# Performance work log

Measured on AMD Instinct MI355X. Metric: run time of the kernel, lower is better.

The kernel has to match this reference:

```python
import jax, jax.numpy as jnp
import numpy as np

EPS = 1e-5  # torch BatchNorm2d default eps


def _conv(x, w, b, pad):
    y = jax.lax.conv_general_dilated(
        x, w, window_strides=(1, 1), padding=[(pad, pad), (pad, pad)],
        dimension_numbers=('NCHW', 'OIHW', 'NCHW'))
    return y + b[None, :, None, None]


def _bn_train(x, gamma, beta):
    # training-mode BatchNorm2d: biased batch statistics over (N,H,W)
    m = jnp.mean(x, axis=(0, 2, 3), keepdims=True)
    v = jnp.var(x, axis=(0, 2, 3), keepdims=True)
    xn = (x - m) * jax.lax.rsqrt(v + EPS)
    return xn * gamma[None, :, None, None] + beta[None, :, None, None]


def _ncc(s, t):
    # Vectorized equivalent of the per-pixel double loop.
    # ncc[b,0,i,j] = mean(tt * ss / (tt_std * ss_std)) over (C,th,tw)
    #             = sum(tt * s_sub) / (N * tt_std * ss_std)   (since sum(tt)=0)
    b, c, sh, sw = s.shape
    th, tw = t.shape[2], t.shape[3]
    N = c * th * tw
    tt = t - jnp.mean(t, axis=(1, 2, 3), keepdims=True)
    # torch.std is unbiased (divides by N-1)
    tt_std = jnp.sqrt(jnp.sum(tt * tt, axis=(1, 2, 3), keepdims=True) / (N - 1))

    # cross[b] = valid correlation of s[b] with its own template tt[b]
    def per_sample(si, ti):
        return jax.lax.conv_general_dilated(
            si[None], ti[None], (1, 1), 'VALID',
            dimension_numbers=('NCHW', 'OIHW', 'NCHW'))[0]  # (1,h,w)

    cross = jax.vmap(per_sample)(s, tt)  # (b,1,h,w)

    # per-window mean/std of s via box-filter conv over all C channels jointly
    box = jnp.ones((1, c, th, tw), dtype=s.dtype)
    win_sum = jax.lax.conv_general_dilated(
        s, box, (1, 1), 'VALID', dimension_numbers=('NCHW', 'OIHW', 'NCHW'))
    win_sqsum = jax.lax.conv_general_dilated(
        s * s, box, (1, 1), 'VALID', dimension_numbers=('NCHW', 'OIHW', 'NCHW'))
    win_mean = win_sum / N
    ss_var = jnp.maximum(win_sqsum - N * win_mean * win_mean, 0.0) / (N - 1)
    ss_std = jnp.sqrt(ss_var)

    return cross / (N * tt_std * ss_std)  # (b,1,h,w)


def reference(s, t, w1, b1, g1, be1, w2, b2, g2, be2,
              w3, b3, g3, be3, w4, b4):
    s = _bn_train(_conv(s, w1, b1, pad=1), g1, be1)
    t = _bn_train(_conv(t, w2, b2, pad=1), g2, be2)
    ncc = _ncc(s, t)
    x = _bn_train(_conv(ncc, w3, b3, pad=0), g3, be3)
    x = jax.nn.relu(x)
    return _conv(x, w4, b4, pad=0)  # (b,2,h,w)


def setup_inputs() -> dict:
    key = jax.random.key(0)
    ks = jax.random.split(key, 12)
    C = 256
    inp = {
        's': jax.random.normal(ks[0], (16, C, 64, 64), jnp.float32),
        't': jax.random.normal(ks[1], (16, C, 16, 16), jnp.float32),
        'w1': jax.random.normal(ks[2], (C, C, 3, 3), jnp.float32) * 0.02,
        'b1': jax.random.normal(ks[3], (C,), jnp.float32) * 0.02,
        'g1': jnp.ones((C,), jnp.float32),
        'be1': jnp.zeros((C,), jnp.float32),
        'w2': jax.random.normal(ks[4], (C, C, 3, 3), jnp.float32) * 0.02,
        'b2': jax.random.normal(ks[5], (C,), jnp.float32) * 0.02,
        'g2': jnp.ones((C,), jnp.float32),
        'be2': jnp.zeros((C,), jnp.float32),
        'w3': jax.random.normal(ks[6], (1, 1, 1, 1), jnp.float32),
        'b3': jax.random.normal(ks[7], (1,), jnp.float32) * 0.02,
        'g3': jnp.ones((1,), jnp.float32),
        'be3': jnp.zeros((1,), jnp.float32),
        'w4': jax.random.normal(ks[8], (2, 1, 1, 1), jnp.float32),
        'b4': jax.random.normal(ks[9], (2,), jnp.float32) * 0.02,
    }
    return inp
```

## Files before the change

kernel.cpp:

```cpp
#include <hip/hip_runtime.h>
#include <hip/hip_bf16.h>

#define EPSV 1e-5f

constexpr int B_ = 16, C_ = 256;
constexpr int OHW_ = 49 * 49;
constexpr int NTOT = 256 * 16 * 16;
constexpr int GROUPS = 32, CPERG = 8;

typedef short bf16x8 __attribute__((ext_vector_type(8)));
typedef float f32x4 __attribute__((ext_vector_type(4)));

constexpr size_t OFF_S1 = 0;
constexpr size_t SZ_S1  = (size_t)16 * 256 * 4096;
constexpr size_t OFF_T2 = OFF_S1 + SZ_S1;
constexpr size_t SZ_T2  = (size_t)16 * 256 * 256;
constexpr size_t OFF_ST = OFF_T2 + SZ_T2;
constexpr size_t OFF_Z  = OFF_ST + 2048;
constexpr size_t OFF_C  = OFF_Z + 131072;
constexpr size_t SPC_BYTES = (size_t)16 * 66 * 66 * 256 * 2;
constexpr size_t TPC_BYTES = (size_t)16 * 18 * 18 * 256 * 2;
constexpr size_t WR_BYTES  = (size_t)9 * 256 * 256 * 2;
constexpr size_t CPOFF = 0;
constexpr size_t NCOFF = CPOFF + (size_t)GROUPS * 16 * OHW_;
constexpr size_t SATOFF = NCOFF + (size_t)16 * OHW_;

__device__ __forceinline__ void gload_lds16(const void* g, void* l) {
    __builtin_amdgcn_global_load_lds((const __attribute__((address_space(1))) unsigned int*)g,
                                     (__attribute__((address_space(3))) unsigned int*)l,
                                     16, 0, 0);
}

template<int W>
__device__ __forceinline__ void pad_body(int bid, const float* __restrict__ in,
                                         __hip_bfloat16* __restrict__ outp, float* tile)
{
    constexpr int PW = W + 2;
    int icg = bid & 3; bid >>= 2;
    int yp = bid % PW; bid /= PW;
    int b = bid;
    int ic0 = icg * 64;
    int tid = threadIdx.x;
    bool interior = (yp >= 1 && yp <= W);
    if (interior) {
        int y = yp - 1;
        for (int idx = tid; idx < 64 * W; idx += 256) {
            int i = idx / W, x = idx % W;
            tile[i * (W + 1) + x] = in[(((size_t)(b * C_ + ic0 + i)) * W + y) * W + x];
        }
    }
    __syncthreads();
    for (int idx = tid; idx < PW * 16; idx += 256) {
        int xp = idx >> 4, i4 = idx & 15;
        ushort4 v = make_ushort4(0, 0, 0, 0);
        if (interior && xp >= 1 && xp <= W) {
            #pragma unroll
            for (int k = 0; k < 4; ++k) {
                __hip_bfloat16 h = __float2bfloat16(tile[(i4 * 4 + k) * (W + 1) + xp - 1]);
                reinterpret_cast<unsigned short*>(&v)[k] = *reinterpret_cast<unsigned short*>(&h);
            }
        }
        *reinterpret_cast<ushort4*>(&outp[(((size_t)(b * PW) + yp) * PW + xp) * 256 + ic0 + i4 * 4]) = v;
    }
}

__global__ __launch_bounds__(256)
void pad_all(const float* __restrict__ s, const float* __restrict__ t,
             __hip_bfloat16* __restrict__ SPc, __hip_bfloat16* __restrict__ TPc,
             const float* __restrict__ w1, const float* __restrict__ w2,
             __hip_bfloat16* __restrict__ wr1, __hip_bfloat16* __restrict__ wr2)
{
    __shared__ float tile[64 * 65];
    constexpr int NP1 = 16 * 66 * 4, NP2 = 16 * 18 * 4;
    int bid = blockIdx.x;
    if (bid < NP1) { pad_body<64>(bid, s, SPc, tile); return; }
    bid -= NP1;
    if (bid < NP2) { pad_body<16>(bid, t, TPc, tile); return; }
    bid -= NP2;
    const float* w = (bid < 256) ? w1 : w2;
    __hip_bfloat16* wr = (bid < 256) ? wr1 : wr2;
    int idx = (bid & 255) * 256 + threadIdx.x;
    const float* src = w + (size_t)idx * 9;
    #pragma unroll
    for (int t_ = 0; t_ < 9; ++t_)
        wr[(size_t)t_ * 65536 + idx] = __float2bfloat16(src[t_]);
}

template<int W>
__device__ __forceinline__ void conv_body(
    int logical,
    const __hip_bfloat16* __restrict__ SPc, const __hip_bfloat16* __restrict__ Wr,
    const float* __restrict__ bias, float* __restrict__ out,
    float* __restrict__ csum, float* __restrict__ csq,
    __hip_bfloat16* A_lds, __hip_bfloat16* B_lds)
{
    constexpr int PW = W + 2;
    constexpr int NPIX = W * W;
    constexpr int NT = NPIX / 128;
    int nt = logical % NT; logical /= NT;
    int mt = logical & 1;  logical >>= 1;
    int b  = logical;
    int tid = threadIdx.x;
    int lane = tid & 63;
    int wv = tid >> 6, wm = wv >> 1, wn = wv & 1;
    int oc0 = mt * 128, p0 = nt * 128;

    f32x4 acc[4][4];
    #pragma unroll
    for (int i = 0; i < 4; ++i)
        #pragma unroll
        for (int j = 0; j < 4; ++j)
            #pragma unroll
            for (int r = 0; r < 4; ++r) acc[i][j][r] = 0.f;

    const bf16x8* Af = reinterpret_cast<const bf16x8*>(A_lds);
    const bf16x8* Bf = reinterpret_cast<const bf16x8*>(B_lds);
    int colb = lane >> 4;
    int rA = lane & 15;

    for (int kc = 0; kc < 72; ++kc) {
        int tap = kc >> 3, icc = kc & 7;
        int ic0 = icc * 32;
        int dy = tap / 3, dx = tap - dy * 3;
        __syncthreads();
        #pragma unroll
        for (int it = 0; it < 2; ++it) {
            int sIdx = tid + it * 256;
            int row = sIdx >> 2, seg = sIdx & 3;
            const __hip_bfloat16* srcA =
                Wr + ((size_t)(tap * 256 + oc0 + row)) * 256 + ic0 + seg * 8;
            gload_lds16(srcA, &A_lds[sIdx * 8]);
            int p = p0 + row;
            int y = p / W, x = p % W;
            const __hip_bfloat16* srcB =
                SPc + (((size_t)(b * PW + y + dy)) * PW + x + dx) * 256 + ic0 + seg * 8;
            gload_lds16(srcB, &B_lds[sIdx * 8]);
        }
        asm volatile("s_waitcnt vmcnt(0)" ::: "memory");
        __syncthreads();

        bf16x8 a[4], bb[4];
        #pragma unroll
        for (int mi = 0; mi < 4; ++mi)
            a[mi] = Af[(wm * 64 + mi * 16 + rA) * 4 + colb];
        #pragma unroll
        for (int ni = 0; ni < 4; ++ni)
            bb[ni] = Bf[(wn * 64 + ni * 16 + rA) * 4 + colb];
        #pragma unroll
        for (int mi = 0; mi < 4; ++mi)
            #pragma unroll
            for (int ni = 0; ni < 4; ++ni)
                acc[mi][ni] = __builtin_amdgcn_mfma_f32_16x16x32_bf16(
                    a[mi], bb[ni], acc[mi][ni], 0, 0, 0);
    }

    #pragma unroll
    for (int mi = 0; mi < 4; ++mi) {
        int ocb = oc0 + wm * 64 + mi * 16 + colb * 4;
        #pragma unroll
        for (int r = 0; r < 4; ++r) {
            int oc = ocb + r;
            float bv = bias[oc];
            float* orow = out + ((size_t)(b * C_ + oc)) * NPIX;
            float s_oc = 0.f, q_oc = 0.f;
            #pragma unroll
            for (int ni = 0; ni < 4; ++ni) {
                int px = p0 + wn * 64 + ni * 16 + rA;
                float v = acc[mi][ni][r] + bv;
                orow[px] = v;
                s_oc += v; q_oc += v * v;
            }
            #pragma unroll
            for (int m_ = 1; m_ < 16; m_ <<= 1) {
                s_oc += __shfl_xor(s_oc, m_);
                q_oc += __shfl_xor(q_oc, m_);
            }
            if (rA == 0) {
                atomicAdd(&csum[oc], s_oc);
                atomicAdd(&csq[oc], q_oc);
            }
        }
    }
}

__global__ __launch_bounds__(256)
void conv_all(const __hip_bfloat16* __restrict__ SPc, const __hip_bfloat16* __restrict__ Wr1,
              const float* __restrict__ b1, float* __restrict__ S1,
              float* __restrict__ CHS1, float* __restrict__ CHQ1,
              const __hip_bfloat16* __restrict__ TPc, const __hip_bfloat16* __restrict__ Wr2,
              const float* __restrict__ b2, float* __restrict__ T2,
              float* __restrict__ CHS2, float* __restrict__ CHQ2)
{
    __shared__ __hip_bfloat16 A_lds[4096];
    __shared__ __hip_bfloat16 B_lds[4096];
    int bid = blockIdx.x;
    if (bid < 64) {
        conv_body<16>(bid, TPc, Wr2, b2, T2, CHS2, CHQ2, A_lds, B_lds);
    } else {
        int l = bid - 64;
        int logical = (l & 7) * 128 + (l >> 3);
        conv_body<64>(logical, SPc, Wr1, b1, S1, CHS1, CHQ1, A_lds, B_lds);
    }
}

__device__ inline void blk_reduce2(float& a, float& q, int tid) {
    #pragma unroll
    for (int off = 32; off > 0; off >>= 1) {
        a += __shfl_down(a, off);
        q += __shfl_down(q, off);
    }
    __shared__ float ra[4], rq[4];
    if ((tid & 63) == 0) { ra[tid >> 6] = a; rq[tid >> 6] = q; }
    __syncthreads();
    if (tid == 0) { a = ra[0] + ra[1] + ra[2] + ra[3]; q = rq[0] + rq[1] + rq[2] + rq[3]; }
}

__global__ __launch_bounds__(256)
void bn_t2_stats(float* __restrict__ T2, const float* __restrict__ csum,
                 const float* __restrict__ csq, const float* __restrict__ g2,
                 const float* __restrict__ be2, float* __restrict__ tmean,
                 float* __restrict__ ttstd)
{
    __shared__ float SC[256], SH[256];
    int b = blockIdx.x, tid = threadIdx.x;
    {
        float m = csum[tid] * (1.f / 4096.f);
        float v = csq[tid] * (1.f / 4096.f) - m * m;
        float sc = rsqrtf(v + EPSV) * g2[tid];
        SC[tid] = sc; SH[tid] = be2[tid] - m * sc;
    }
    __syncthreads();
    float4* p = reinterpret_cast<float4*>(T2 + (size_t)b * NTOT);
    float s = 0.f, q = 0.f;
    for (int i4 = tid; i4 < NTOT / 4; i4 += 256) {
        int c = i4 >> 6;
        float sc = SC[c], sh = SH[c];
        float4 v = p[i4];
        v.x = v.x * sc + sh; v.y = v.y * sc + sh;
        v.z = v.z * sc + sh; v.w = v.w * sc + sh;
        s += v.x + v.y + v.z + v.w;
        q += v.x * v.x + v.y * v.y + v.z * v.z + v.w * v.w;
        p[i4] = v;
    }
    blk_reduce2(s, q, tid);
    if (tid == 0) {
        float m = s / (float)NTOT;
        tmean[b] = m;
        ttstd[b] = sqrtf(fmaxf(q - (float)NTOT * m * m, 0.f) / (float)(NTOT - 1));
    }
}

__global__ __launch_bounds__(256, 2)
void cross_v3(const float* __restrict__ s1, const float* __restrict__ t2,
              const float* __restrict__ csum, const float* __restrict__ csq,
              const float* __restrict__ g1, const float* __restrict__ be1,
              float* __restrict__ cpart, float* __restrict__ z)
{
    __shared__ float4 spl4[1024];
    __shared__ float tpl[256];
    __shared__ float red[4][64][49];

    int g = blockIdx.x & (GROUPS - 1);
    int b = blockIdx.x / GROUPS;
    int tid = threadIdx.x;
    int phase = tid >> 6;
    int lane = tid & 63;
    int i = lane;
    int i_ld = i < 49 ? i : 48;

    float acc[49];
    #pragma unroll
    for (int j = 0; j < 49; ++j) acc[j] = 0.f;
    float4 zs[4], zq[4];
    #pragma unroll
    for (int k = 0; k < 4; ++k) {
        zs[k] = make_float4(0.f, 0.f, 0.f, 0.f);
        zq[k] = make_float4(0.f, 0.f, 0.f, 0.f);
    }

    #pragma unroll 1
    for (int cc = 0; cc < CPERG; ++cc) {
        int c = g * CPERG + cc;
        float m = csum[c] * (1.f / 65536.f);
        float v = csq[c] * (1.f / 65536.f) - m * m;
        float sc = rsqrtf(v + EPSV) * g1[c];
        float sh = be1[c] - m * sc;
        __syncthreads();
        const float4* sp4 = reinterpret_cast<const float4*>(s1 + ((size_t)(b * C_ + c)) * 4096);
        #pragma unroll
        for (int k = 0; k < 4; ++k) {
            int gidx = tid + k * 256;
            float4 val = sp4[gidx];
            val.x = val.x * sc + sh; val.y = val.y * sc + sh;
            val.z = val.z * sc + sh; val.w = val.w * sc + sh;
            zs[k].x += val.x; zs[k].y += val.y; zs[k].z += val.z; zs[k].w += val.w;
            zq[k].x += val.x * val.x; zq[k].y += val.y * val.y;
            zq[k].z += val.z * val.z; zq[k].w += val.w * val.w;
            int row = gidx >> 4, jg = gidx & 15;
            spl4[row * 16 + (jg ^ (row & 7))] = val;
        }
        tpl[tid] = t2[((size_t)(b * C_ + c)) * 256 + tid];
        __syncthreads();
        #pragma unroll 1
        for (int tyl = 0; tyl < 4; ++tyl) {
            int ty = phase * 4 + tyl;
            int row = i_ld + ty;
            float r_[64];
            #pragma unroll
            for (int jg = 0; jg < 16; ++jg) {
                float4 v4 = spl4[row * 16 + (jg ^ (row & 7))];
                r_[jg * 4 + 0] = v4.x; r_[jg * 4 + 1] = v4.y;
                r_[jg * 4 + 2] = v4.z; r_[jg * 4 + 3] = v4.w;
            }
            float tt[16];
            const float4* tp4 = reinterpret_cast<const float4*>(&tpl[ty * 16]);
            #pragma unroll
            for (int k = 0; k < 4; ++k) {
                float4 tv = tp4[k];
                tt[k * 4 + 0] = tv.x; tt[k * 4 + 1] = tv.y;
                tt[k * 4 + 2] = tv.z; tt[k * 4 + 3] = tv.w;
            }
            #pragma unroll
            for (int tx = 0; tx < 16; ++tx)
                #pragma unroll
                for (int j = 0; j < 49; ++j)
                    acc[j] += tt[tx] * r_[j + tx];
        }
    }
    #pragma unroll
    for (int k = 0; k < 4; ++k) {
        int pxb = (tid + k * 256) * 4;
        float* zb  = z + (size_t)b * 4096 + pxb;
        float* z2b = z + 65536 + (size_t)b * 4096 + pxb;
        atomicAdd(&zb[0], zs[k].x);  atomicAdd(&zb[1], zs[k].y);
        atomicAdd(&zb[2], zs[k].z);  atomicAdd(&zb[3], zs[k].w);
        atomicAdd(&z2b[0], zq[k].x); atomicAdd(&z2b[1], zq[k].y);
        atomicAdd(&z2b[2], zq[k].z); atomicAdd(&z2b[3], zq[k].w);
    }
    __syncthreads();
    if (i < 49) {
        #pragma unroll
        for (int j = 0; j < 49; ++j) red[phase][i][j] = acc[j];
    }
    __syncthreads();
    float* dst = cpart + ((size_t)(g * B_ + b)) * OHW_;
    for (int e = tid; e < OHW_; e += 256) {
        int ii = e / 49, jj = e - ii * 49;
        dst[e] = red[0][ii][jj] + red[1][ii][jj] + red[2][ii][jj] + red[3][ii][jj];
    }
}

__global__ __launch_bounds__(256)
void sat_kernel(const float* __restrict__ zin, float* __restrict__ sat)
{
    __shared__ float t[65][66];
    int pl = blockIdx.x;
    int tid = threadIdx.x;
    const float* src = zin + (size_t)pl * 4096;
    for (int idx = tid; idx < 4096; idx += 256) {
        int y = idx >> 6, x = idx & 63;
        t[y + 1][x + 1] = src[idx];
    }
    for (int idx = tid; idx < 65; idx += 256) { t[0][idx] = 0.f; t[idx][0] = 0.f; }
    __syncthreads();
    if (tid < 64) {
        float run = 0.f;
        for (int x = 1; x <= 64; ++x) { run += t[tid + 1][x]; t[tid + 1][x] = run; }
    }
    __syncthreads();
    if (tid < 64) {
        float run = 0.f;
        for (int y = 1; y <= 64; ++y) { run += t[y][tid + 1]; t[y][tid + 1] = run; }
    }
    __syncthreads();
    float* dst = sat + (size_t)pl * 4225;
    for (int idx = tid; idx < 4225; idx += 256) {
        int r = idx / 65, c = idx % 65;
        dst[idx] = t[r][c];
    }
}

__global__ __launch_bounds__(256)
void ncc_kernel(const float* __restrict__ cpart, const float* __restrict__ sat,
                const float* __restrict__ tmean, const float* __restrict__ ttstd,
                float* __restrict__ ncc, float* __restrict__ s3)
{
    int idx = blockIdx.x * 256 + threadIdx.x;
    float val = 0.f;
    if (idx < B_ * OHW_) {
        int b = idx / OHW_, r = idx - b * OHW_;
        int i = r / 49, j = r - i * 49;
        float cr = 0.f;
        #pragma unroll 4
        for (int g = 0; g < GROUPS; ++g) cr += cpart[((size_t)(g * B_ + b)) * OHW_ + r];
        const float* sz = sat + (size_t)b * 4225;
        const float* sq = sat + (size_t)(16 + b) * 4225;
        int a00 = i * 65 + j, a01 = i * 65 + j + 16;
        int a10 = (i + 16) * 65 + j, a11 = (i + 16) * 65 + j + 16;
        float wsum = sz[a11] - sz[a01] - sz[a10] + sz[a00];
        float wq   = sq[a11] - sq[a01] - sq[a10] + sq[a00];
        float crosst = cr - tmean[b] * wsum;
        float ssvar = fmaxf(wq - wsum * wsum * (1.f / 65536.f), 0.f) * (1.f / 65535.f);
        float ssstd = sqrtf(ssvar);
        val = crosst / (65536.f * ttstd[b] * ssstd);
        ncc[idx] = val;
    }
    float s = val, q = val * val;
    blk_reduce2(s, q, threadIdx.x);
    if (threadIdx.x == 0) { atomicAdd(&s3[0], s); atomicAdd(&s3[1], q); }
}

__global__ __launch_bounds__(256)
void final_kernel(const float* __restrict__ ncc, const float* __restrict__ s3,
                  const float* __restrict__ w3, const float* __restrict__ b3,
                  const float* __restrict__ g3, const float* __restrict__ be3,
                  const float* __restrict__ w4, const float* __restrict__ b4,
                  float* __restrict__ out)
{
    int idx = blockIdx.x * 256 + threadIdx.x;
    if (idx >= B_ * OHW_) return;
    constexpr float M = (float)(B_ * OHW_);
    float mn = s3[0] / M;
    float vn = s3[1] / M - mn * mn;
    float W3 = w3[0], B3 = b3[0];
    float my = W3 * mn + B3;
    float vy = W3 * W3 * vn;
    float sc = rsqrtf(vy + EPSV) * g3[0];
    float y = (W3 * ncc[idx] + B3 - my) * sc + be3[0];
    float h = fmaxf(y, 0.f);
    int b = idx / OHW_, r = idx - b * OHW_;
    out[((size_t)(b * 2 + 0)) * OHW_ + r] = h * w4[0] + b4[0];
    out[((size_t)(b * 2 + 1)) * OHW_ + r] = h * w4[1] + b4[1];
}

extern "C" void kernel_launch(void* const* d_in, const int* in_sizes, int n_in,
                              void* d_out, int out_size, void* d_ws, size_t ws_size,
                              hipStream_t stream)
{
    const float* s   = (const float*)d_in[0];
    const float* t   = (const float*)d_in[1];
    const float* w1  = (const float*)d_in[2];
    const float* b1  = (const float*)d_in[3];
    const float* g1  = (const float*)d_in[4];
    const float* be1 = (const float*)d_in[5];
    const float* w2  = (const float*)d_in[6];
    const float* b2  = (const float*)d_in[7];
    const float* g2  = (const float*)d_in[8];
    const float* be2 = (const float*)d_in[9];
    const float* w3  = (const float*)d_in[10];
    const float* b3  = (const float*)d_in[11];
    const float* g3  = (const float*)d_in[12];
    const float* be3 = (const float*)d_in[13];
    const float* w4  = (const float*)d_in[14];
    const float* b4  = (const float*)d_in[15];

    float* ws = (float*)d_ws;
    float* S1 = ws + OFF_S1;
    float* T2 = ws + OFF_T2;
    float* ST = ws + OFF_ST;
    float* CHS1 = ST + 0;
    float* CHQ1 = ST + 256;
    float* CHS2 = ST + 512;
    float* CHQ2 = ST + 768;
    float* S3   = ST + 1024;
    float* TM   = ST + 1040;
    float* TSD  = ST + 1056;
    float* Z    = ws + OFF_Z;

    char* Cb = (char*)(ws + OFF_C);
    __hip_bfloat16* SPc = (__hip_bfloat16*)Cb;
    __hip_bfloat16* TPc = (__hip_bfloat16*)(Cb + SPC_BYTES);
    __hip_bfloat16* Wr1 = (__hip_bfloat16*)(Cb + SPC_BYTES + TPC_BYTES);
    __hip_bfloat16* Wr2 = (__hip_bfloat16*)(Cb + SPC_BYTES + TPC_BYTES + WR_BYTES);
    float* Cf = (float*)Cb;
    float* CP  = Cf + CPOFF;
    float* NC  = Cf + NCOFF;
    float* SAT = Cf + SATOFF;

    hipMemsetAsync(ST, 0, (2048 + 131072) * sizeof(float), stream);

    pad_all<<<dim3(16 * 66 * 4 + 16 * 18 * 4 + 512), dim3(256), 0, stream>>>(
        s, t, SPc, TPc, w1, w2, Wr1, Wr2);

    conv_all<<<dim3(64 + 1024), dim3(256), 0, stream>>>(SPc, Wr1, b1, S1, CHS1, CHQ1,
                                                        TPc, Wr2, b2, T2, CHS2, CHQ2);

    bn_t2_stats<<<dim3(16), dim3(256), 0, stream>>>(T2, CHS2, CHQ2, g2, be2, TM, TSD);

    cross_v3<<<dim3(16 * GROUPS), dim3(256), 0, stream>>>(S1, T2, CHS1, CHQ1, g1, be1, CP, Z);
    sat_kernel<<<dim3(32), dim3(256), 0, stream>>>(Z, SAT);
    ncc_kernel<<<dim3(151), dim3(256), 0, stream>>>(CP, SAT, TM, TSD, NC, S3);
    final_kernel<<<dim3(151), dim3(256), 0, stream>>>(NC, S3, w3, b3, g3, be3, w4, b4, (float*)d_out);
}
```

Measured before the change: 438.9 us.

## Rewrite conv GEMM as 256x256 tile, 8-wave, double-buffered swizzled LDS pipeline

Replaces the 128x128, 4-wave conv kernel, which waited on a full load before every K step, with a 256x256 output tile computed by 8 waves. Global-to-LDS loads for the next K step are double-buffered and interleaved with MFMA quadrants using partial vmcnt waits and raw barriers. LDS rows are XOR-swizzled to avoid bank conflicts, and s_setprio raises priority during the MFMA blocks. The trade is 128KB of dynamic LDS per block, many more accumulator registers, and only 272 blocks, which may leave the grid poorly balanced across CUs.

```diff
diff --git a/kernel.cpp b/kernel.cpp
--- a/kernel.cpp
+++ b/kernel.cpp
@@ -87,86 +87,163 @@
 }
 
 template<int W>
-__device__ __forceinline__ void conv_body(
-    int logical,
+__device__ __forceinline__ void conv8p_body(
+    int bb, int nt,
     const __hip_bfloat16* __restrict__ SPc, const __hip_bfloat16* __restrict__ Wr,
     const float* __restrict__ bias, float* __restrict__ out,
-    float* __restrict__ csum, float* __restrict__ csq,
-    __hip_bfloat16* A_lds, __hip_bfloat16* B_lds)
+    float* __restrict__ csum, float* __restrict__ csq, char* smem)
 {
     constexpr int PW = W + 2;
     constexpr int NPIX = W * W;
-    constexpr int NT = NPIX / 128;
-    int nt = logical % NT; logical /= NT;
-    int mt = logical & 1;  logical >>= 1;
-    int b  = logical;
+    constexpr int LOG2W = (W == 64) ? 6 : 4;
     int tid = threadIdx.x;
     int lane = tid & 63;
-    int wv = tid >> 6, wm = wv >> 1, wn = wv & 1;
-    int oc0 = mt * 128, p0 = nt * 128;
-
-    f32x4 acc[4][4];
-    #pragma unroll
-    for (int i = 0; i < 4; ++i)
+    int wv = tid >> 6;
+    int wm = wv >> 2, wn = wv & 3;
+    int rA = lane & 15, colb = lane >> 4;
+
+    f32x4 acc[8][4];
+    #pragma unroll
+    for (int i = 0; i < 8; ++i)
         #pragma unroll
         for (int j = 0; j < 4; ++j)
             #pragma unroll
             for (int r = 0; r < 4; ++r) acc[i][j][r] = 0.f;
 
-    const bf16x8* Af = reinterpret_cast<const bf16x8*>(A_lds);
-    const bf16x8* Bf = reinterpret_cast<const bf16x8*>(B_lds);
-    int colb = lane >> 4;
-    int rA = lane & 15;
-
-    for (int kc = 0; kc < 72; ++kc) {
-        int tap = kc >> 3, icc = kc & 7;
-        int ic0 = icc * 32;
+    int row_s[2], gs_s[2];
+    #pragma unroll
+    for (int k = 0; k < 2; ++k) {
+        int si = tid + k * 512;
+        int row = si >> 3, g = si & 7;
+        row_s[k] = row; gs_s[k] = g ^ (row & 7);
+    }
+
+    auto Abase = [&](int s, int half) { return smem + s * 32768 + half * 16384; };
+    auto Bbase = [&](int s, int half) { return smem + 65536 + s * 32768 + half * 16384; };
+
+    auto stageA = [&](int s, int half, int kt) {
+        int tap = kt >> 2, icc = kt & 3;
+        char* dst = Abase(s, half);
+        #pragma unroll
+        for (int k = 0; k < 2; ++k) {
+            const __hip_bfloat16* src =
+                Wr + ((size_t)(tap * 256 + half * 128 + row_s[k])) * 256 + icc * 64 + gs_s[k] * 8;
+            gload_lds16(src, dst + (tid + k * 512) * 16);
+        }
+    };
+    auto stageB = [&](int s, int half, int kt) {
+        int tap = kt >> 2, icc = kt & 3;
         int dy = tap / 3, dx = tap - dy * 3;
-        __syncthreads();
-        #pragma unroll
-        for (int it = 0; it < 2; ++it) {
-            int sIdx = tid + it * 256;
-            int row = sIdx >> 2, seg = sIdx & 3;
-            const __hip_bfloat16* srcA =
-                Wr + ((size_t)(tap * 256 + oc0 + row)) * 256 + ic0 + seg * 8;
-            gload_lds16(srcA, &A_lds[sIdx * 8]);
-            int p = p0 + row;
-            int y = p / W, x = p % W;
-            const __hip_bfloat16* srcB =
-                SPc + (((size_t)(b * PW + y + dy)) * PW + x + dx) * 256 + ic0 + seg * 8;
-            gload_lds16(srcB, &B_lds[sIdx * 8]);
-        }
-        asm volatile("s_waitcnt vmcnt(0)" ::: "memory");
-        __syncthreads();
-
-        bf16x8 a[4], bb[4];
-        #pragma unroll
-        for (int mi = 0; mi < 4; ++mi)
-            a[mi] = Af[(wm * 64 + mi * 16 + rA) * 4 + colb];
-        #pragma unroll
-        for (int ni = 0; ni < 4; ++ni)
-            bb[ni] = Bf[(wn * 64 + ni * 16 + rA) * 4 + colb];
-        #pragma unroll
-        for (int mi = 0; mi < 4; ++mi)
-            #pragma unroll
-            for (int ni = 0; ni < 4; ++ni)
-                acc[mi][ni] = __builtin_amdgcn_mfma_f32_16x16x32_bf16(
-                    a[mi], bb[ni], acc[mi][ni], 0, 0, 0);
-    }
-
-    #pragma unroll
-    for (int mi = 0; mi < 4; ++mi) {
-        int ocb = oc0 + wm * 64 + mi * 16 + colb * 4;
+        char* dst = Bbase(s, half);
+        #pragma unroll
+        for (int k = 0; k < 2; ++k) {
+            int row = row_s[k];
+            int gy = nt * (256 >> LOG2W) + ((half * 128 + row) >> LOG2W) + dy;
+            int gx = (row & (W - 1)) + dx;
+            const __hip_bfloat16* src =
+                SPc + (((size_t)(bb * PW + gy)) * PW + gx) * 256 + icc * 64 + gs_s[k] * 8;
+            gload_lds16(src, dst + (tid + k * 512) * 16);
+        }
+    };
+
+    bf16x8 a[4][2];
+    bf16x8 bfr[2][2][2];
+    auto loadA = [&](int s, int half) {
+        const bf16x8* Av = (const bf16x8*)Abase(s, half);
+        #pragma unroll
+        for (int mi = 0; mi < 4; ++mi) {
+            int rl = wm * 64 + mi * 16 + rA;
+            #pragma unroll
+            for (int ks = 0; ks < 2; ++ks)
+                a[mi][ks] = Av[rl * 8 + ((ks * 4 + colb) ^ (rA & 7))];
+        }
+    };
+    auto loadB0 = [&](int s) {
+        const bf16x8* Bv = (const bf16x8*)Bbase(s, 0);
+        #pragma unroll
+        for (int ni = 0; ni < 2; ++ni) {
+            int rl = wn * 32 + ni * 16 + rA;
+            #pragma unroll
+            for (int ks = 0; ks < 2; ++ks)
+                bfr[0][ni][ks] = Bv[rl * 8 + ((ks * 4 + colb) ^ (rA & 7))];
+        }
+    };
+    auto loadB1 = [&](int s) {
+        const bf16x8* Bv = (const bf16x8*)Bbase(s, 1);
+        #pragma unroll
+        for (int ni = 0; ni < 2; ++ni) {
+            int rl = wn * 32 + ni * 16 + rA;
+            #pragma unroll
+            for (int ks = 0; ks < 2; ++ks)
+                bfr[1][ni][ks] = Bv[rl * 8 + ((ks * 4 + colb) ^ (rA & 7))];
+        }
+    };
+
+    #define QUAD(mh, nh)                                                            \
+        __builtin_amdgcn_s_setprio(1);                                              \
+        _Pragma("unroll")                                                           \
+        for (int mi = 0; mi < 4; ++mi)                                              \
+            _Pragma("unroll")                                                       \
+            for (int ni = 0; ni < 2; ++ni)                                          \
+                _Pragma("unroll")                                                   \
+                for (int ks = 0; ks < 2; ++ks)                                      \
+                    acc[(mh)*4+mi][(nh)*2+ni] = __builtin_amdgcn_mfma_f32_16x16x32_bf16( \
+                        a[mi][ks], bfr[nh][ni][ks], acc[(mh)*4+mi][(nh)*2+ni], 0,0,0);   \
+        __builtin_amdgcn_s_setprio(0);
+
+    stageA(0, 0, 0); stageB(0, 0, 0); stageB(0, 1, 0); stageA(0, 1, 0);
+    asm volatile("s_waitcnt vmcnt(4)" ::: "memory");
+    asm volatile("s_barrier" ::: "memory");
+
+    for (int kt = 0; kt < 36; ++kt) {
+        int s = kt & 1, sn = s ^ 1;
+        bool st = (kt < 35);
+        int nkt = kt + 1;
+        loadA(s, 0); loadB0(s);
+        if (st) {
+            stageA(sn, 0, nkt);
+            asm volatile("s_waitcnt vmcnt(4)" ::: "memory");
+        } else {
+            asm volatile("s_waitcnt vmcnt(2)" ::: "memory");
+        }
+        asm volatile("s_barrier" ::: "memory");
+        QUAD(0, 0)
+        loadB1(s);
+        if (st) {
+            stageB(sn, 0, nkt);
+            asm volatile("s_waitcnt vmcnt(4)" ::: "memory");
+        } else {
+            asm volatile("s_waitcnt vmcnt(0)" ::: "memory");
+        }
+        asm volatile("s_barrier" ::: "memory");
+        QUAD(0, 1)
+        loadA(s, 1);
+        if (st) stageB(sn, 1, nkt);
+        asm volatile("s_barrier" ::: "memory");
+        QUAD(1, 0)
+        if (st) {
+            stageA(sn, 1, nkt);
+            asm volatile("s_waitcnt vmcnt(4)" ::: "memory");
+        }
+        asm volatile("s_barrier" ::: "memory");
+        QUAD(1, 1)
+    }
+    #undef QUAD
+
+    int p0g = nt * 256;
+    #pragma unroll
+    for (int mi = 0; mi < 8; ++mi) {
+        int oc = (mi >> 2) * 128 + wm * 64 + (mi & 3) * 16 + colb * 4;
         #pragma unroll
         for (int r = 0; r < 4; ++r) {
-            int oc = ocb + r;
-            float bv = bias[oc];
-            float* orow = out + ((size_t)(b * C_ + oc)) * NPIX;
+            int ocr = oc + r;
+            float bv = bias[ocr];
+            float* orow = out + ((size_t)(bb * C_ + ocr)) * NPIX;
             float s_oc = 0.f, q_oc = 0.f;
             #pragma unroll
-            for (int ni = 0; ni < 4; ++ni) {
-                int px = p0 + wn * 64 + ni * 16 + rA;
-                float v = acc[mi][ni][r] + bv;
+            for (int nj = 0; nj < 4; ++nj) {
+                int px = p0g + (nj >> 1) * 128 + wn * 32 + (nj & 1) * 16 + rA;
+                float v = acc[mi][nj][r] + bv;
                 orow[px] = v;
                 s_oc += v; q_oc += v * v;
             }
@@ -176,30 +253,29 @@
                 q_oc += __shfl_xor(q_oc, m_);
             }
             if (rA == 0) {
-                atomicAdd(&csum[oc], s_oc);
-                atomicAdd(&csq[oc], q_oc);
+                atomicAdd(&csum[ocr], s_oc);
+                atomicAdd(&csq[ocr], q_oc);
             }
         }
     }
 }
 
-__global__ __launch_bounds__(256)
-void conv_all(const __hip_bfloat16* __restrict__ SPc, const __hip_bfloat16* __restrict__ Wr1,
-              const float* __restrict__ b1, float* __restrict__ S1,
-              float* __restrict__ CHS1, float* __restrict__ CHQ1,
-              const __hip_bfloat16* __restrict__ TPc, const __hip_bfloat16* __restrict__ Wr2,
-              const float* __restrict__ b2, float* __restrict__ T2,
-              float* __restrict__ CHS2, float* __restrict__ CHQ2)
-{
-    __shared__ __hip_bfloat16 A_lds[4096];
-    __shared__ __hip_bfloat16 B_lds[4096];
+__global__ __launch_bounds__(512, 2)
+void conv8p(const __hip_bfloat16* __restrict__ SPc, const __hip_bfloat16* __restrict__ Wr1,
+            const float* __restrict__ b1, float* __restrict__ S1,
+            float* __restrict__ CHS1, float* __restrict__ CHQ1,
+            const __hip_bfloat16* __restrict__ TPc, const __hip_bfloat16* __restrict__ Wr2,
+            const float* __restrict__ b2, float* __restrict__ T2,
+            float* __restrict__ CHS2, float* __restrict__ CHQ2)
+{
+    extern __shared__ char smem[];
     int bid = blockIdx.x;
-    if (bid < 64) {
-        conv_body<16>(bid, TPc, Wr2, b2, T2, CHS2, CHQ2, A_lds, B_lds);
+    if (bid < 16) {
+        conv8p_body<16>(bid, 0, TPc, Wr2, b2, T2, CHS2, CHQ2, smem);
     } else {
-        int l = bid - 64;
-        int logical = (l & 7) * 128 + (l >> 3);
-        conv_body<64>(logical, SPc, Wr1, b1, S1, CHS1, CHQ1, A_lds, B_lds);
+        int l = bid - 16;
+        int logical = (l & 7) * 32 + (l >> 3);
+        conv8p_body<64>(logical >> 4, logical & 15, SPc, Wr1, b1, S1, CHS1, CHQ1, smem);
     }
 }
 
@@ -482,8 +558,10 @@
     pad_all<<<dim3(16 * 66 * 4 + 16 * 18 * 4 + 512), dim3(256), 0, stream>>>(
         s, t, SPc, TPc, w1, w2, Wr1, Wr2);
 
-    conv_all<<<dim3(64 + 1024), dim3(256), 0, stream>>>(SPc, Wr1, b1, S1, CHS1, CHQ1,
-                                                        TPc, Wr2, b2, T2, CHS2, CHQ2);
+    (void)hipFuncSetAttribute((const void*)conv8p,
+                              hipFuncAttributeMaxDynamicSharedMemorySize, 131072);
+    conv8p<<<dim3(16 + 256), dim3(512), 131072, stream>>>(SPc, Wr1, b1, S1, CHS1, CHQ1,
+                                                          TPc, Wr2, b2, T2, CHS2, CHQ2);
 
     bn_t2_stats<<<dim3(16), dim3(256), 0, stream>>>(T2, CHS2, CHQ2, g2, be2, TM, TSD);
 
```

Result: slower. 456.1 us (+3.9%).

## Store conv1 output as bf16 and fold template BN stats into cross kernel

Applied to the files above, without the earlier changes.

The large conv1 output S1 is now written in bf16 instead of fp32, which halves its write traffic in the conv kernel and its read traffic in the cross-correlation kernel. The separate bn_t2_stats launch is removed. Its per-sample mean/std computation now runs in 16 extra blocks of the cross kernel, and the T2 normalization is applied on the fly when the template is loaded, so T2 is no longer rewritten. The cost is bf16 rounding of S1 before BN and the NCC statistics, which could affect accuracy.

```diff
diff --git a/kernel.cpp b/kernel.cpp
--- a/kernel.cpp
+++ b/kernel.cpp
@@ -10,10 +10,11 @@
 
 typedef short bf16x8 __attribute__((ext_vector_type(8)));
 typedef float f32x4 __attribute__((ext_vector_type(4)));
+typedef unsigned short ushort8v __attribute__((ext_vector_type(8)));
 
 constexpr size_t OFF_S1 = 0;
-constexpr size_t SZ_S1  = (size_t)16 * 256 * 4096;
-constexpr size_t OFF_T2 = OFF_S1 + SZ_S1;
+constexpr size_t SZ_S1F = (size_t)16 * 256 * 4096 / 2;
+constexpr size_t OFF_T2 = OFF_S1 + SZ_S1F;
 constexpr size_t SZ_T2  = (size_t)16 * 256 * 256;
 constexpr size_t OFF_ST = OFF_T2 + SZ_T2;
 constexpr size_t OFF_Z  = OFF_ST + 2048;
@@ -30,6 +31,9 @@
                                      (__attribute__((address_space(3))) unsigned int*)l,
                                      16, 0, 0);
 }
+
+__device__ __forceinline__ void store_val(float* p, float v) { *p = v; }
+__device__ __forceinline__ void store_val(__hip_bfloat16* p, float v) { *p = __float2bfloat16(v); }
 
 template<int W>
 __device__ __forceinline__ void pad_body(int bid, const float* __restrict__ in,
@@ -86,11 +90,11 @@
         wr[(size_t)t_ * 65536 + idx] = __float2bfloat16(src[t_]);
 }
 
-template<int W>
+template<int W, typename OT>
 __device__ __forceinline__ void conv_body(
     int logical,
     const __hip_bfloat16* __restrict__ SPc, const __hip_bfloat16* __restrict__ Wr,
-    const float* __restrict__ bias, float* __restrict__ out,
+    const float* __restrict__ bias, OT* __restrict__ out,
     float* __restrict__ csum, float* __restrict__ csq,
     __hip_bfloat16* A_lds, __hip_bfloat16* B_lds)
 {
@@ -161,13 +165,13 @@
         for (int r = 0; r < 4; ++r) {
             int oc = ocb + r;
             float bv = bias[oc];
-            float* orow = out + ((size_t)(b * C_ + oc)) * NPIX;
+            OT* orow = out + ((size_t)(b * C_ + oc)) * NPIX;
             float s_oc = 0.f, q_oc = 0.f;
             #pragma unroll
             for (int ni = 0; ni < 4; ++ni) {
                 int px = p0 + wn * 64 + ni * 16 + rA;
                 float v = acc[mi][ni][r] + bv;
-                orow[px] = v;
+                store_val(&orow[px], v);
                 s_oc += v; q_oc += v * v;
             }
             #pragma unroll
@@ -185,7 +189,7 @@
 
 __global__ __launch_bounds__(256)
 void conv_all(const __hip_bfloat16* __restrict__ SPc, const __hip_bfloat16* __restrict__ Wr1,
-              const float* __restrict__ b1, float* __restrict__ S1,
+              const float* __restrict__ b1, __hip_bfloat16* __restrict__ S1,
               float* __restrict__ CHS1, float* __restrict__ CHQ1,
               const __hip_bfloat16* __restrict__ TPc, const __hip_bfloat16* __restrict__ Wr2,
               const float* __restrict__ b2, float* __restrict__ T2,
@@ -195,11 +199,11 @@
     __shared__ __hip_bfloat16 B_lds[4096];
     int bid = blockIdx.x;
     if (bid < 64) {
-        conv_body<16>(bid, TPc, Wr2, b2, T2, CHS2, CHQ2, A_lds, B_lds);
+        conv_body<16, float>(bid, TPc, Wr2, b2, T2, CHS2, CHQ2, A_lds, B_lds);
     } else {
         int l = bid - 64;
         int logical = (l & 7) * 128 + (l >> 3);
-        conv_body<64>(logical, SPc, Wr1, b1, S1, CHS1, CHQ1, A_lds, B_lds);
+        conv_body<64, __hip_bfloat16>(logical, SPc, Wr1, b1, S1, CHS1, CHQ1, A_lds, B_lds);
     }
 }
 
@@ -215,54 +219,52 @@
     if (tid == 0) { a = ra[0] + ra[1] + ra[2] + ra[3]; q = rq[0] + rq[1] + rq[2] + rq[3]; }
 }
 
-__global__ __launch_bounds__(256)
-void bn_t2_stats(float* __restrict__ T2, const float* __restrict__ csum,
-                 const float* __restrict__ csq, const float* __restrict__ g2,
-                 const float* __restrict__ be2, float* __restrict__ tmean,
-                 float* __restrict__ ttstd)
-{
-    __shared__ float SC[256], SH[256];
-    int b = blockIdx.x, tid = threadIdx.x;
-    {
-        float m = csum[tid] * (1.f / 4096.f);
-        float v = csq[tid] * (1.f / 4096.f) - m * m;
-        float sc = rsqrtf(v + EPSV) * g2[tid];
-        SC[tid] = sc; SH[tid] = be2[tid] - m * sc;
-    }
-    __syncthreads();
-    float4* p = reinterpret_cast<float4*>(T2 + (size_t)b * NTOT);
-    float s = 0.f, q = 0.f;
-    for (int i4 = tid; i4 < NTOT / 4; i4 += 256) {
-        int c = i4 >> 6;
-        float sc = SC[c], sh = SH[c];
-        float4 v = p[i4];
-        v.x = v.x * sc + sh; v.y = v.y * sc + sh;
-        v.z = v.z * sc + sh; v.w = v.w * sc + sh;
-        s += v.x + v.y + v.z + v.w;
-        q += v.x * v.x + v.y * v.y + v.z * v.z + v.w * v.w;
-        p[i4] = v;
-    }
-    blk_reduce2(s, q, tid);
-    if (tid == 0) {
-        float m = s / (float)NTOT;
-        tmean[b] = m;
-        ttstd[b] = sqrtf(fmaxf(q - (float)NTOT * m * m, 0.f) / (float)(NTOT - 1));
-    }
-}
-
 __global__ __launch_bounds__(256, 2)
-void cross_v3(const float* __restrict__ s1, const float* __restrict__ t2,
-              const float* __restrict__ csum, const float* __restrict__ csq,
+void cross_v4(const __hip_bfloat16* __restrict__ s1, const float* __restrict__ t2,
+              const float* __restrict__ cs1, const float* __restrict__ cq1,
               const float* __restrict__ g1, const float* __restrict__ be1,
-              float* __restrict__ cpart, float* __restrict__ z)
-{
+              const float* __restrict__ cs2, const float* __restrict__ cq2,
+              const float* __restrict__ g2, const float* __restrict__ be2,
+              float* __restrict__ cpart, float* __restrict__ z,
+              float* __restrict__ tmean, float* __restrict__ ttstd)
+{
+    int tid = threadIdx.x;
+    if (blockIdx.x >= 16 * GROUPS) {
+        __shared__ float SC[256], SH[256];
+        int b = blockIdx.x - 16 * GROUPS;
+        {
+            float m = cs2[tid] * (1.f / 4096.f);
+            float v = cq2[tid] * (1.f / 4096.f) - m * m;
+            float sc = rsqrtf(v + EPSV) * g2[tid];
+            SC[tid] = sc; SH[tid] = be2[tid] - m * sc;
+        }
+        __syncthreads();
+        const float4* p = reinterpret_cast<const float4*>(t2 + (size_t)b * NTOT);
+        float s = 0.f, q = 0.f;
+        for (int i4 = tid; i4 < NTOT / 4; i4 += 256) {
+            int c = i4 >> 6;
+            float sc = SC[c], sh = SH[c];
+            float4 v = p[i4];
+            float vx = v.x * sc + sh, vy = v.y * sc + sh;
+            float vz = v.z * sc + sh, vw = v.w * sc + sh;
+            s += vx + vy + vz + vw;
+            q += vx * vx + vy * vy + vz * vz + vw * vw;
+        }
+        blk_reduce2(s, q, tid);
+        if (tid == 0) {
+            float m = s / (float)NTOT;
+            tmean[b] = m;
+            ttstd[b] = sqrtf(fmaxf(q - (float)NTOT * m * m, 0.f) / (float)(NTOT - 1));
+        }
+        return;
+    }
+
     __shared__ float4 spl4[1024];
     __shared__ float tpl[256];
     __shared__ float red[4][64][49];
 
     int g = blockIdx.x & (GROUPS - 1);
     int b = blockIdx.x / GROUPS;
-    int tid = threadIdx.x;
     int phase = tid >> 6;
     int lane = tid & 63;
     int i = lane;
@@ -271,35 +273,42 @@
     float acc[49];
     #pragma unroll
     for (int j = 0; j < 49; ++j) acc[j] = 0.f;
-    float4 zs[4], zq[4];
-    #pragma unroll
-    for (int k = 0; k < 4; ++k) {
-        zs[k] = make_float4(0.f, 0.f, 0.f, 0.f);
-        zq[k] = make_float4(0.f, 0.f, 0.f, 0.f);
-    }
+    float zsA[2][8], zqA[2][8];
+    #pragma unroll
+    for (int k = 0; k < 2; ++k)
+        #pragma unroll
+        for (int e = 0; e < 8; ++e) { zsA[k][e] = 0.f; zqA[k][e] = 0.f; }
 
     #pragma unroll 1
     for (int cc = 0; cc < CPERG; ++cc) {
         int c = g * CPERG + cc;
-        float m = csum[c] * (1.f / 65536.f);
-        float v = csq[c] * (1.f / 65536.f) - m * m;
-        float sc = rsqrtf(v + EPSV) * g1[c];
-        float sh = be1[c] - m * sc;
+        float m1 = cs1[c] * (1.f / 65536.f);
+        float v1 = cq1[c] * (1.f / 65536.f) - m1 * m1;
+        float sc1 = rsqrtf(v1 + EPSV) * g1[c];
+        float sh1 = be1[c] - m1 * sc1;
+        float m2 = cs2[c] * (1.f / 4096.f);
+        float v2 = cq2[c] * (1.f / 4096.f) - m2 * m2;
+        float sc2 = rsqrtf(v2 + EPSV) * g2[c];
+        float sh2 = be2[c] - m2 * sc2;
         __syncthreads();
-        const float4* sp4 = reinterpret_cast<const float4*>(s1 + ((size_t)(b * C_ + c)) * 4096);
-        #pragma unroll
-        for (int k = 0; k < 4; ++k) {
-            int gidx = tid + k * 256;
-            float4 val = sp4[gidx];
-            val.x = val.x * sc + sh; val.y = val.y * sc + sh;
-            val.z = val.z * sc + sh; val.w = val.w * sc + sh;
-            zs[k].x += val.x; zs[k].y += val.y; zs[k].z += val.z; zs[k].w += val.w;
-            zq[k].x += val.x * val.x; zq[k].y += val.y * val.y;
-            zq[k].z += val.z * val.z; zq[k].w += val.w * val.w;
-            int row = gidx >> 4, jg = gidx & 15;
-            spl4[row * 16 + (jg ^ (row & 7))] = val;
-        }
-        tpl[tid] = t2[((size_t)(b * C_ + c)) * 256 + tid];
+        const ushort8v* sp8 = reinterpret_cast<const ushort8v*>(s1 + ((size_t)(b * C_ + c)) * 4096);
+        #pragma unroll
+        for (int k = 0; k < 2; ++k) {
+            int idx = tid + k * 256;
+            ushort8v u = sp8[idx];
+            float f[8];
+            #pragma unroll
+            for (int e = 0; e < 8; ++e) {
+                f[e] = __uint_as_float(((unsigned)u[e]) << 16) * sc1 + sh1;
+                zsA[k][e] += f[e];
+                zqA[k][e] += f[e] * f[e];
+            }
+            int row = idx >> 3;
+            int gp = (idx & 7) * 2;
+            spl4[row * 16 + (gp ^ (row & 7))] = make_float4(f[0], f[1], f[2], f[3]);
+            spl4[row * 16 + ((gp + 1) ^ (row & 7))] = make_float4(f[4], f[5], f[6], f[7]);
+        }
+        tpl[tid] = t2[((size_t)(b * C_ + c)) * 256 + tid] * sc2 + sh2;
         __syncthreads();
         #pragma unroll 1
         for (int tyl = 0; tyl < 4; ++tyl) {
@@ -328,14 +337,15 @@
         }
     }
     #pragma unroll
-    for (int k = 0; k < 4; ++k) {
-        int pxb = (tid + k * 256) * 4;
+    for (int k = 0; k < 2; ++k) {
+        int pxb = (tid + k * 256) * 8;
         float* zb  = z + (size_t)b * 4096 + pxb;
         float* z2b = z + 65536 + (size_t)b * 4096 + pxb;
-        atomicAdd(&zb[0], zs[k].x);  atomicAdd(&zb[1], zs[k].y);
-        atomicAdd(&zb[2], zs[k].z);  atomicAdd(&zb[3], zs[k].w);
-        atomicAdd(&z2b[0], zq[k].x); atomicAdd(&z2b[1], zq[k].y);
-        atomicAdd(&z2b[2], zq[k].z); atomicAdd(&z2b[3], zq[k].w);
+        #pragma unroll
+        for (int e = 0; e < 8; ++e) {
+            atomicAdd(&zb[e], zsA[k][e]);
+            atomicAdd(&z2b[e], zqA[k][e]);
+        }
     }
     __syncthreads();
     if (i < 49) {
@@ -455,7 +465,7 @@
     const float* b4  = (const float*)d_in[15];
 
     float* ws = (float*)d_ws;
-    float* S1 = ws + OFF_S1;
+    __hip_bfloat16* S1b = (__hip_bfloat16*)(ws + OFF_S1);
     float* T2 = ws + OFF_T2;
     float* ST = ws + OFF_ST;
     float* CHS1 = ST + 0;
@@ -482,12 +492,12 @@
     pad_all<<<dim3(16 * 66 * 4 + 16 * 18 * 4 + 512), dim3(256), 0, stream>>>(
         s, t, SPc, TPc, w1, w2, Wr1, Wr2);
 
-    conv_all<<<dim3(64 + 1024), dim3(256), 0, stream>>>(SPc, Wr1, b1, S1, CHS1, CHQ1,
+    conv_all<<<dim3(64 + 1024), dim3(256), 0, stream>>>(SPc, Wr1, b1, S1b, CHS1, CHQ1,
                                                         TPc, Wr2, b2, T2, CHS2, CHQ2);
 
-    bn_t2_stats<<<dim3(16), dim3(256), 0, stream>>>(T2, CHS2, CHQ2, g2, be2, TM, TSD);
-
-    cross_v3<<<dim3(16 * GROUPS), dim3(256), 0, stream>>>(S1, T2, CHS1, CHQ1, g1, be1, CP, Z);
+    cross_v4<<<dim3(16 * GROUPS + 16), dim3(256), 0, stream>>>(
+        S1b, T2, CHS1, CHQ1, g1, be1, CHS2, CHQ2, g2, be2, CP, Z, TM, TSD);
+
     sat_kernel<<<dim3(32), dim3(256), 0, stream>>>(Z, SAT);
     ncc_kernel<<<dim3(151), dim3(256), 0, stream>>>(CP, SAT, TM, TSD, NC, S3);
     final_kernel<<<dim3(151), dim3(256), 0, stream>>>(NC, S3, w3, b3, g3, be3, w4, b4, (float*)d_out);
```

Result: slower. 485.9 us (+10.7%).

## Double-buffer conv LDS tiles, XOR-swizzle LDS layout, and set occupancy bound

Applied to the files above, without the earlier changes.

The implicit-GEMM conv loop now loads the next K-chunk into a second LDS buffer while MFMAs run on the current one, which removes one barrier per iteration and hides global-to-LDS latency. The LDS row segments are XOR-swizzled by row so the fragment reads avoid bank conflicts. Launch bounds now request 4 blocks per CU. In exchange, LDS per block doubles to 32 KB, and the occupancy hint may cap registers.

```diff
diff --git a/kernel.cpp b/kernel.cpp
--- a/kernel.cpp
+++ b/kernel.cpp
@@ -92,7 +92,7 @@
     const __hip_bfloat16* __restrict__ SPc, const __hip_bfloat16* __restrict__ Wr,
     const float* __restrict__ bias, float* __restrict__ out,
     float* __restrict__ csum, float* __restrict__ csq,
-    __hip_bfloat16* A_lds, __hip_bfloat16* B_lds)
+    __hip_bfloat16 (&A_lds)[2][4096], __hip_bfloat16 (&B_lds)[2][4096])
 {
     constexpr int PW = W + 2;
     constexpr int NPIX = W * W;
@@ -113,45 +113,65 @@
             #pragma unroll
             for (int r = 0; r < 4; ++r) acc[i][j][r] = 0.f;
 
-    const bf16x8* Af = reinterpret_cast<const bf16x8*>(A_lds);
-    const bf16x8* Bf = reinterpret_cast<const bf16x8*>(B_lds);
     int colb = lane >> 4;
     int rA = lane & 15;
-
-    for (int kc = 0; kc < 72; ++kc) {
+    int s_row[2], s_seg[2];
+    #pragma unroll
+    for (int it = 0; it < 2; ++it) {
+        int sIdx = tid + it * 256;
+        s_row[it] = sIdx >> 2;
+        s_seg[it] = (sIdx & 3) ^ (s_row[it] & 3);
+    }
+
+    auto STAGE = [&](int buf, int kc) {
         int tap = kc >> 3, icc = kc & 7;
         int ic0 = icc * 32;
         int dy = tap / 3, dx = tap - dy * 3;
-        __syncthreads();
         #pragma unroll
         for (int it = 0; it < 2; ++it) {
             int sIdx = tid + it * 256;
-            int row = sIdx >> 2, seg = sIdx & 3;
+            int row = s_row[it], sw = s_seg[it];
             const __hip_bfloat16* srcA =
-                Wr + ((size_t)(tap * 256 + oc0 + row)) * 256 + ic0 + seg * 8;
-            gload_lds16(srcA, &A_lds[sIdx * 8]);
+                Wr + ((size_t)(tap * 256 + oc0 + row)) * 256 + ic0 + sw * 8;
+            gload_lds16(srcA, &A_lds[buf][sIdx * 8]);
             int p = p0 + row;
             int y = p / W, x = p % W;
             const __hip_bfloat16* srcB =
-                SPc + (((size_t)(b * PW + y + dy)) * PW + x + dx) * 256 + ic0 + seg * 8;
-            gload_lds16(srcB, &B_lds[sIdx * 8]);
-        }
-        asm volatile("s_waitcnt vmcnt(0)" ::: "memory");
-        __syncthreads();
-
+                SPc + (((size_t)(b * PW + y + dy)) * PW + x + dx) * 256 + ic0 + sw * 8;
+            gload_lds16(srcB, &B_lds[buf][sIdx * 8]);
+        }
+    };
+
+    STAGE(0, 0);
+    asm volatile("s_waitcnt vmcnt(0)" ::: "memory");
+    __syncthreads();
+
+    for (int kc = 0; kc < 72; ++kc) {
+        int cur = kc & 1;
+        if (kc + 1 < 72) STAGE(cur ^ 1, kc + 1);
+
+        const bf16x8* Af = reinterpret_cast<const bf16x8*>(&A_lds[cur][0]);
+        const bf16x8* Bf = reinterpret_cast<const bf16x8*>(&B_lds[cur][0]);
         bf16x8 a[4], bb[4];
         #pragma unroll
-        for (int mi = 0; mi < 4; ++mi)
-            a[mi] = Af[(wm * 64 + mi * 16 + rA) * 4 + colb];
-        #pragma unroll
-        for (int ni = 0; ni < 4; ++ni)
-            bb[ni] = Bf[(wn * 64 + ni * 16 + rA) * 4 + colb];
+        for (int mi = 0; mi < 4; ++mi) {
+            int rowA = wm * 64 + mi * 16 + rA;
+            a[mi] = Af[rowA * 4 + (colb ^ (rowA & 3))];
+        }
+        #pragma unroll
+        for (int ni = 0; ni < 4; ++ni) {
+            int rowB = wn * 64 + ni * 16 + rA;
+            bb[ni] = Bf[rowB * 4 + (colb ^ (rowB & 3))];
+        }
         #pragma unroll
         for (int mi = 0; mi < 4; ++mi)
             #pragma unroll
             for (int ni = 0; ni < 4; ++ni)
                 acc[mi][ni] = __builtin_amdgcn_mfma_f32_16x16x32_bf16(
                     a[mi], bb[ni], acc[mi][ni], 0, 0, 0);
+
+        asm volatile("s_waitcnt vmcnt(0)" ::: "memory");
+        __syncthreads();
     }
 
     #pragma unroll
@@ -183,7 +203,7 @@
     }
 }
 
-__global__ __launch_bounds__(256)
+__global__ __launch_bounds__(256, 4)
 void conv_all(const __hip_bfloat16* __restrict__ SPc, const __hip_bfloat16* __restrict__ Wr1,
               const float* __restrict__ b1, float* __restrict__ S1,
               float* __restrict__ CHS1, float* __restrict__ CHQ1,
@@ -191,8 +211,8 @@
               const float* __restrict__ b2, float* __restrict__ T2,
               float* __restrict__ CHS2, float* __restrict__ CHQ2)
 {
-    __shared__ __hip_bfloat16 A_lds[4096];
-    __shared__ __hip_bfloat16 B_lds[4096];
+    __shared__ __hip_bfloat16 A_lds[2][4096];
+    __shared__ __hip_bfloat16 B_lds[2][4096];
     int bid = blockIdx.x;
     if (bid < 64) {
         conv_body<16>(bid, TPc, Wr2, b2, T2, CHS2, CHQ2, A_lds, B_lds);
```

New measurement: 455.0 us. +3.7%, slower.
